# Kernel tuning notes

Hardware: AMD Instinct MI355X
Metric: run time of the kernel (lower is better)

Reference implementation:

```python
import jax, jax.numpy as jnp
import numpy as np

VOCAB, TAGS, EDIM, HDIM = 50000, 9, 256, 512
H = HDIM // 2  # per-direction LSTM hidden
B, S = 64, 512


def setup_inputs() -> dict:
    key = jax.random.key(0)
    ks = jax.random.split(key, 16)
    sc = 0.05
    inp = {
        'sentence_batch': jax.random.randint(ks[0], (B, S), 0, VOCAB),
        'tags_batch': jax.random.randint(ks[1], (B, S), 0, TAGS),
        'mask': jnp.ones((B, S), dtype=bool),
        'emb': jax.random.normal(ks[2], (VOCAB, EDIM), jnp.float32) * sc,
        'w_ih_f': jax.random.normal(ks[3], (4 * H, EDIM), jnp.float32) * sc,
        'w_hh_f': jax.random.normal(ks[4], (4 * H, H), jnp.float32) * sc,
        'b_ih_f': jnp.zeros((4 * H,), jnp.float32),
        'b_hh_f': jnp.zeros((4 * H,), jnp.float32),
        'w_ih_b': jax.random.normal(ks[5], (4 * H, EDIM), jnp.float32) * sc,
        'w_hh_b': jax.random.normal(ks[6], (4 * H, H), jnp.float32) * sc,
        'b_ih_b': jnp.zeros((4 * H,), jnp.float32),
        'b_hh_b': jnp.zeros((4 * H,), jnp.float32),
        'w_out': jax.random.normal(ks[7], (TAGS, HDIM), jnp.float32) * sc,
        'b_out': jnp.zeros((TAGS,), jnp.float32),
        'start_trans': jax.random.uniform(ks[8], (TAGS,), jnp.float32, -0.1, 0.1),
        'end_trans': jax.random.uniform(ks[9], (TAGS,), jnp.float32, -0.1, 0.1),
        'trans': jax.random.uniform(ks[10], (TAGS, TAGS), jnp.float32, -0.1, 0.1),
    }
    return inp


def _lstm_dir(x, w_ih, w_hh, b_ih, b_hh):
    # x: [B,S,E] -> [B,S,H], torch gate order (i,f,g,o)
    b, h = x.shape[0], w_hh.shape[1]
    xg = jnp.einsum('bse,ge->bsg', x, w_ih) + b_ih + b_hh  # precompute input gates

    def step(carry, xg_t):
        hprev, cprev = carry
        g = xg_t + hprev @ w_hh.T
        i, f, gg, o = jnp.split(g, 4, axis=-1)
        c = jax.nn.sigmoid(f) * cprev + jax.nn.sigmoid(i) * jnp.tanh(gg)
        hnew = jax.nn.sigmoid(o) * jnp.tanh(c)
        return (hnew, c), hnew

    init = (jnp.zeros((b, h), x.dtype), jnp.zeros((b, h), x.dtype))
    _, hs = jax.lax.scan(step, init, jnp.swapaxes(xg, 0, 1))
    return jnp.swapaxes(hs, 0, 1)


def _crf_nll(emissions, tags, mask, start_trans, end_trans, trans):
    # emissions [B,S,T], tags [B,S], mask [B,S] bool. torchcrf llh, reduction='mean'.
    b, s, t = emissions.shape
    mf = mask.astype(emissions.dtype)
    # numerator score
    em_sc = jnp.take_along_axis(emissions, tags[..., None], axis=-1)[..., 0]  # [B,S]
    tr_sc = trans[tags[:, :-1], tags[:, 1:]]  # [B,S-1]
    score = start_trans[tags[:, 0]] + em_sc[:, 0]
    score = score + jnp.sum((tr_sc + em_sc[:, 1:]) * mf[:, 1:], axis=-1)
    seq_ends = jnp.sum(mask.astype(jnp.int32), axis=1) - 1
    last_tags = jnp.take_along_axis(tags, seq_ends[:, None], axis=1)[:, 0]
    score = score + end_trans[last_tags]
    # partition via forward algorithm (scan over time)
    alpha0 = start_trans[None, :] + emissions[:, 0]  # [B,T]

    def step(alpha, inputs):
        em_t, m_t = inputs  # [B,T], [B]
        nxt = jax.nn.logsumexp(alpha[:, :, None] + trans[None] + em_t[:, None, :], axis=1)
        alpha = jnp.where(m_t[:, None], nxt, alpha)
        return alpha, None

    em_tm = jnp.swapaxes(emissions[:, 1:], 0, 1)  # [S-1,B,T]
    m_tm = jnp.swapaxes(mask[:, 1:], 0, 1)  # [S-1,B]
    alpha, _ = jax.lax.scan(step, alpha0, (em_tm, m_tm))
    logZ = jax.nn.logsumexp(alpha + end_trans[None, :], axis=-1)
    llh = score - logZ
    return -jnp.mean(llh)


def reference(sentence_batch, tags_batch, mask, emb,
              w_ih_f, w_hh_f, b_ih_f, b_hh_f,
              w_ih_b, w_hh_b, b_ih_b, b_hh_b,
              w_out, b_out, start_trans, end_trans, trans):
    x = emb[sentence_batch]  # [B,S,E]
    hf = _lstm_dir(x, w_ih_f, w_hh_f, b_ih_f, b_hh_f)
    hb = _lstm_dir(x[:, ::-1], w_ih_b, w_hh_b, b_ih_b, b_hh_b)[:, ::-1]
    feats = jnp.concatenate([hf, hb], axis=-1) @ w_out.T + b_out  # [B,S,TAGS]
    return _crf_nll(feats, tags_batch, mask, start_trans, end_trans, trans)
```

## Files before the change

kernel.cpp:

```cpp
#include <hip/hip_runtime.h>
#include <stdint.h>

typedef unsigned short u16;
typedef __attribute__((ext_vector_type(4))) float f32x4;
typedef __attribute__((ext_vector_type(8))) short short8;
typedef __attribute__((ext_vector_type(8))) int v8i;

#define OFF_BIAS   ((size_t)0)
#define OFF_WFRAG  ((size_t)8192)
#define OFF_HHIST  ((size_t)1048576)
#define OFF_FEATS  ((size_t)34603008)
#define OFF_XG     ((size_t)37748736)
#define OFF_XBF    ((size_t)171966464)
#define OFF_WBF    ((size_t)188743680)

__device__ __forceinline__ float bf2f(u16 h) {
  union { uint32_t u; float f; } v; v.u = ((uint32_t)h) << 16; return v.f;
}
__device__ __forceinline__ float bfh(uint32_t wrd, int hh) {
  return bf2f((u16)(wrd >> (16 * hh)));
}
__device__ __forceinline__ uint32_t cvtpk_bf16(float lo, float hi) {
  uint32_t r;
  asm("v_cvt_pk_bf16_f32 %0, %1, %2" : "=v"(r) : "v"(lo), "v"(hi));
  return r;
}
__device__ __forceinline__ uint32_t f2u(float f) {
  union { float f; uint32_t u; } v; v.f = f; return v.u;
}
__device__ __forceinline__ float u2f(uint32_t u) {
  union { uint32_t u; float f; } v; v.u = u; return v.f;
}
__device__ __forceinline__ float pl32_lo(float a, float b) {
  auto pr = __builtin_amdgcn_permlane32_swap(f2u(a), f2u(b), false, false);
  return u2f(((const uint32_t*)&pr)[0]);
}
__device__ __forceinline__ float pl32_hi(float a, float b) {
  auto pr = __builtin_amdgcn_permlane32_swap(f2u(a), f2u(b), false, false);
  return u2f(((const uint32_t*)&pr)[1]);
}
__device__ __forceinline__ short8 pack8(f32x4 a, f32x4 b) {
  union { short8 s; uint32_t u[4]; } r;
  r.u[0] = cvtpk_bf16(a[0], a[1]);
  r.u[1] = cvtpk_bf16(a[2], a[3]);
  r.u[2] = cvtpk_bf16(b[0], b[1]);
  r.u[3] = cvtpk_bf16(b[2], b[3]);
  return r.s;
}

__global__ void bias_kernel(const float* __restrict__ bihf, const float* __restrict__ bhhf,
                            const float* __restrict__ bihb, const float* __restrict__ bhhb,
                            float* __restrict__ bias) {
  int n = blockIdx.x * 256 + threadIdx.x;
  if (n < 1024) bias[n] = bihf[n] + bhhf[n];
  else          bias[n] = bihb[n - 1024] + bhhb[n - 1024];
}

__global__ void __launch_bounds__(256) pack_kernel(
    const int* __restrict__ sent, const float* __restrict__ emb,
    const float* __restrict__ wihf, const float* __restrict__ wihb,
    u16* __restrict__ xbf, u16* __restrict__ wbf)
{
  int gid = blockIdx.x * 256 + threadIdx.x;
  if (gid < 1048576) {
    const int tok = gid >> 5;
    const int c8 = (gid & 31) * 8;
    const int t = sent[tok];
    const float* src = emb + (size_t)t * 256 + c8;
    f32x4 a0 = *(const f32x4*)(src);
    f32x4 a1 = *(const f32x4*)(src + 4);
    *(short8*)(xbf + (size_t)tok * 256 + c8) = pack8(a0, a1);
  } else if (gid < 1114112) {
    const int g2 = gid - 1048576;
    const int row = g2 >> 5;
    const int c8 = (g2 & 31) * 8;
    const float* W = (row < 1024) ? wihf : wihb;
    const float* src = W + (size_t)(row & 1023) * 256 + c8;
    f32x4 a0 = *(const f32x4*)(src);
    f32x4 a1 = *(const f32x4*)(src + 4);
    *(short8*)(wbf + (size_t)row * 256 + c8) = pack8(a0, a1);
  }
}

__global__ void wfrag_prep_kernel(const float* __restrict__ whhf,
                                  const float* __restrict__ whhb,
                                  uint8_t* __restrict__ wfrag) {
  int gid = blockIdx.x * 256 + threadIdx.x;
  const int l    = gid & 63;
  const int kt   = (gid >> 6) & 7;
  const int gate = (gid >> 9) & 3;
  const int ubi  = (gid >> 11) & 1;
  const int w    = (gid >> 12) & 7;
  const int d    = (gid >> 15) & 1;
  const float* W = d ? whhb : whhf;
  const int n = l & 15, q = l >> 4;
  const int row = gate * 256 + w * 32 + ubi * 16 + n;
  uint32_t out[2] = {0u, 0u};
  #pragma unroll
  for (int jj = 0; jj < 4; ++jj) {
    const int k0 = kt * 32 + q * 8 + jj * 2;
    const int k1 = k0 + 1;
    const int u0 = (k0 >> 5) * 32 + (k0 & 1) * 16 + ((k0 & 31) >> 1);
    const int u1 = (k1 >> 5) * 32 + (k1 & 1) * 16 + ((k1 & 31) >> 1);
    const float f0 = W[(size_t)row * 256 + u0] * 16.0f;
    const float f1 = W[(size_t)row * 256 + u1] * 16.0f;
    const int pk = __builtin_amdgcn_cvt_pk_fp8_f32(f0, f1, 0, false);
    out[jj >> 1] |= (uint32_t)(pk & 0xffff) << (16 * (jj & 1));
  }
  const int p = kt >> 2, cc = kt & 3;
  const size_t addr =
      ((((size_t)((d * 8 + w) * 2 + ubi) * 4 + gate) * 2 + p) * 64 + l) * 32 + (size_t)cc * 8;
  *(uint2*)(wfrag + addr) = make_uint2(out[0], out[1]);
}

__global__ void __launch_bounds__(256) xg_gemm_kernel(
    const u16* __restrict__ xbf, const u16* __restrict__ wbf,
    const float* __restrict__ bias, u16* __restrict__ xgf)
{
  extern __shared__ char smem[];
  u16*   Al    = (u16*)smem;
  u16*   Bl    = (u16*)(smem + 34816);
  float* biasl = (float*)(smem + 69632);

  const int tid = threadIdx.x;
  const int d  = blockIdx.x >> 3, u0 = (blockIdx.x & 7) * 32;
  const int g  = blockIdx.y >> 6, qb = (blockIdx.y >> 4) & 3, s0 = (blockIdx.y & 15) * 32;

  if (tid < 128)
    biasl[tid] = bias[d * 1024 + (tid >> 5) * 256 + u0 + (tid & 31)];
  __syncthreads();

  f32x4 acc[4][4];
  #pragma unroll
  for (int i = 0; i < 4; ++i)
    #pragma unroll
    for (int j = 0; j < 4; ++j) acc[i][j] = (f32x4){0.f, 0.f, 0.f, 0.f};

  const int wv = tid >> 6, l = tid & 63;
  const int mh = (wv >> 1) * 64, nh = (wv & 1) * 64;
  const int fr = l & 15, fq = l >> 4;
  const int rr = tid >> 1, c0 = (tid & 1) * 64;

  const int xrow = (g * 16 + qb * 4 + (rr & 3)) * 512 + s0 + (rr >> 2);
  const int wrow = d * 1024 + (rr >> 5) * 256 + u0 + (rr & 31);

  for (int kc = 0; kc < 2; ++kc) {
    const int k0 = kc * 128;
    const u16* as = xbf + (size_t)xrow * 256 + k0 + c0;
    const u16* bs = wbf + (size_t)wrow * 256 + k0 + c0;
    u16* adst = Al + rr * 136 + c0;
    u16* bdst = Bl + rr * 136 + c0;
    #pragma unroll
    for (int gdx = 0; gdx < 8; ++gdx) {
      *(short8*)(adst + gdx * 8) = *(const short8*)(as + gdx * 8);
      *(short8*)(bdst + gdx * 8) = *(const short8*)(bs + gdx * 8);
    }
    __syncthreads();
    #pragma unroll
    for (int ks = 0; ks < 4; ++ks) {
      short8 af[4], bfr[4];
      #pragma unroll
      for (int i = 0; i < 4; ++i)
        af[i] = *(const short8*)(Al + (mh + i * 16 + fr) * 136 + ks * 32 + fq * 8);
      #pragma unroll
      for (int j = 0; j < 4; ++j)
        bfr[j] = *(const short8*)(Bl + (nh + j * 16 + fr) * 136 + ks * 32 + fq * 8);
      #pragma unroll
      for (int i = 0; i < 4; ++i)
        #pragma unroll
        for (int j = 0; j < 4; ++j)
          acc[i][j] = __builtin_amdgcn_mfma_f32_16x16x32_bf16(af[i], bfr[j], acc[i][j], 0, 0, 0);
    }
    __syncthreads();
  }

  const float LOG2E = 1.4426950408889634f;
  const int g0 = nh >> 5;
  const float sA = (g0 == 2) ? (2.0f * LOG2E) : (-LOG2E);
  const int mh4 = mh >> 2;
  const int g8 = g * 2 + (qb >> 1);
  const int qh = qb & 1;
  u16* xbase = xgf + (size_t)(d * 8 + g8) * 4194304;
  #pragma unroll
  for (int i = 0; i < 4; ++i) {
    const int s = s0 + mh4 + i * 4 + fq;
    #pragma unroll
    for (int nsub = 0; nsub < 2; ++nsub) {
      const int j0 = nsub, j1 = nsub + 2;
      const int cA = nh + j0 * 16 + fr, cB = nh + j1 * 16 + fr;
      const int tid2 = (u0 >> 5) * 64 + ((nsub << 1) | qh) * 16 + fr;
      float vA[4], vB[4];
      #pragma unroll
      for (int r = 0; r < 4; ++r) {
        vA[r] = (acc[i][j0][r] + biasl[cA]) * sA;
        vB[r] = (acc[i][j1][r] + biasl[cB]) * (-LOG2E);
      }
      union { short8 s8; uint32_t u[4]; } sv;
      sv.u[0] = cvtpk_bf16(vA[0], vA[1]);
      sv.u[1] = cvtpk_bf16(vA[2], vA[3]);
      sv.u[2] = cvtpk_bf16(vB[0], vB[1]);
      sv.u[3] = cvtpk_bf16(vB[2], vB[3]);
      *(short8*)(xbase + (size_t)s * 8192 + tid2 * 16 + g0 * 4) = sv.s8;
    }
  }
}

template<int CB, int PW>
__device__ __forceinline__ void lstm_step(
    int T, int d, int l, int q, int n, int w,
    const v8i (&wvr)[2][4][2], float (&cst)[4],
    uint4& X0, uint4& X1,
    uint8_t* hx, const u16* xsl, u16* hhb)
{
  const int t_eff = d ? (511 - T) : T;
  const int qh = q & 1;

  int tn = T + 2; if (tn > 511) tn = 511;
  const int sn = d ? (511 - tn) : tn;
  const uint4* pf = (const uint4*)(xsl + (size_t)sn * 8192);
  const uint4 P0 = pf[0], P1 = pf[1];

  const uint8_t* hr = hx + CB * 4224 + (l & 15) * 264 + q * 8;
  const int2 b0 = *(const int2*)(hr +   0);
  const int2 b1 = *(const int2*)(hr +  32);
  const int2 b2 = *(const int2*)(hr +  64);
  const int2 b3 = *(const int2*)(hr +  96);
  const int2 b4 = *(const int2*)(hr + 128);
  const int2 b5 = *(const int2*)(hr + 160);
  const int2 b6 = *(const int2*)(hr + 192);
  const int2 b7 = *(const int2*)(hr + 224);
  const v8i A0 = (v8i){b0.x, b0.y, b1.x, b1.y, b2.x, b2.y, b3.x, b3.y};
  const v8i A1 = (v8i){b4.x, b4.y, b5.x, b5.y, b6.x, b6.y, b7.x, b7.y};

  f32x4 acc[2][4];
  #pragma unroll
  for (int ubi = 0; ubi < 2; ++ubi)
    #pragma unroll
    for (int gate = 0; gate < 4; ++gate) {
      f32x4 a = (f32x4){0.f, 0.f, 0.f, 0.f};
      a = __builtin_amdgcn_mfma_scale_f32_16x16x128_f8f6f4(
              A0, wvr[ubi][gate][0], a, 0, 0, 0, 0x7f7f7f7f, 0, 0x7f7f7f7f);
      a = __builtin_amdgcn_mfma_scale_f32_16x16x128_f8f6f4(
              A1, wvr[ubi][gate][1], a, 0, 0, 0, 0x7f7f7f7f, 0, 0x7f7f7f7f);
      acc[ubi][gate] = a;
    }

  f32x4 accs[4];
  #pragma unroll
  for (int gate = 0; gate < 4; ++gate)
    #pragma unroll
    for (int r = 0; r < 4; ++r)
      accs[gate][r] = pl32_lo(acc[0][gate][r], acc[1][gate][r]);

  const float Sm = -0.0056355275f;
  const float Sg =  0.0112710550f;
  const float K2 =  2.8853900818f;
  float hval[4];
  #pragma unroll
  for (int r = 0; r < 4; ++r) {
    const uint32_t wi = (r < 2) ? X0.x : X0.y;
    const uint32_t wf = (r < 2) ? X0.z : X0.w;
    const uint32_t wg = (r < 2) ? X1.x : X1.y;
    const uint32_t wo = (r < 2) ? X1.z : X1.w;
    const int hp = r & 1;
    const float argi = fmaf(accs[0][r], Sm, bfh(wi, hp));
    const float argf = fmaf(accs[1][r], Sm, bfh(wf, hp));
    const float argg = fmaf(accs[2][r], Sg, bfh(wg, hp));
    const float argo = fmaf(accs[3][r], Sm, bfh(wo, hp));
    const float Ei = __builtin_amdgcn_exp2f(argi);
    const float Ef = __builtin_amdgcn_exp2f(argf);
    const float Eg = __builtin_amdgcn_exp2f(argg);
    const float Eo = __builtin_amdgcn_exp2f(argo);
    const float pf_ = 1.0f + Ef, pi_ = 1.0f + Ei, pg_ = 1.0f + Eg;
    const float P  = pi_ * pg_;
    const float rD = __builtin_amdgcn_rcpf(P * pf_);
    const float num = fmaf(cst[r], P, fmaf(Eg, pf_, -pf_));
    const float c   = num * rD;
    cst[r] = c;
    const float E2 = __builtin_amdgcn_exp2f(c * K2);
    const float rQ = __builtin_amdgcn_rcpf((1.0f + E2) * (1.0f + Eo));
    hval[r] = fmaf(E2, rQ, -rQ);
  }

  float ho[4];
  #pragma unroll
  for (int r = 0; r < 4; ++r) ho[r] = pl32_hi(hval[r], hval[r]);
  if (q < 2) {
    uint8_t* hw = hx + PW * 4224 + w * 32 + 2 * n;
    #pragma unroll
    for (int r = 0; r < 4; ++r) {
      const int pk = __builtin_amdgcn_cvt_pk_fp8_f32(hval[r] * 16.0f,
                                                     ho[r] * 16.0f, 0, false);
      *(u16*)(hw + (q * 4 + r) * 264) = (u16)(pk & 0xffff);
    }
  }

  asm volatile("s_waitcnt lgkmcnt(0)" ::: "memory");
  __builtin_amdgcn_s_barrier();
  __builtin_amdgcn_sched_barrier(0);

  {
    u16* hhs = hhb + (size_t)t_eff * 256;
    const uint32_t pb01 = cvtpk_bf16(hval[0], hval[1]);
    const uint32_t pb23 = cvtpk_bf16(hval[2], hval[3]);
    hhs[(size_t)(qh * 4 + 0) * 131072] = (u16)(pb01 & 0xffffu);
    hhs[(size_t)(qh * 4 + 1) * 131072] = (u16)(pb01 >> 16);
    hhs[(size_t)(qh * 4 + 2) * 131072] = (u16)(pb23 & 0xffffu);
    hhs[(size_t)(qh * 4 + 3) * 131072] = (u16)(pb23 >> 16);
  }

  X0 = P0; X1 = P1;
}

__global__ void __launch_bounds__(512, 2) lstm_kernel(
    const u16* __restrict__ xgf, const uint8_t* __restrict__ wfrag,
    u16* __restrict__ hhist)
{
  __shared__ uint8_t hx[2 * 16 * 264];

  const int tid = threadIdx.x;
  const int bid = blockIdx.x;
  const int d = bid >> 3, g8 = bid & 7;
  const int w = tid >> 6, l = tid & 63;
  const int n = l & 15, q = l >> 4;

  v8i wvr[2][4][2];
  {
    const uint8_t* wb = wfrag + (size_t)(d * 8 + w) * 32768;
    #pragma unroll
    for (int ubi = 0; ubi < 2; ++ubi)
      #pragma unroll
      for (int gate = 0; gate < 4; ++gate)
        #pragma unroll
        for (int p = 0; p < 2; ++p) {
          const uint8_t* src = wb + ((size_t)(((ubi * 4 + gate) * 2 + p) * 64 + l)) * 32;
          const uint4 lo = *(const uint4*)(src);
          const uint4 hi = *(const uint4*)(src + 16);
          wvr[ubi][gate][p] = (v8i){(int)lo.x, (int)lo.y, (int)lo.z, (int)lo.w,
                                    (int)hi.x, (int)hi.y, (int)hi.z, (int)hi.w};
        }
  }

  for (int i = tid; i < 2112; i += 512) ((uint32_t*)hx)[i] = 0u;

  const u16* xsl = xgf + (size_t)(d * 8 + g8) * 4194304 + (size_t)tid * 16;
  float cst[4] = {};
  u16* hhb = hhist + ((size_t)(d * 64 + g8 * 8) * 512) * 256 + (w * 32 + (q >> 1) * 16 + n);

  uint4 X0, X1, Y0, Y1;
  {
    const uint4* p0 = (const uint4*)(xsl + (size_t)(d ? 511 : 0) * 8192);
    X0 = p0[0]; X1 = p0[1];
    const uint4* p1 = (const uint4*)(xsl + (size_t)(d ? 510 : 1) * 8192);
    Y0 = p1[0]; Y1 = p1[1];
  }
  __syncthreads();

  for (int tt = 0; tt < 512; tt += 2) {
    lstm_step<0, 1>(tt,     d, l, q, n, w, wvr, cst, X0, X1, hx, xsl, hhb);
    lstm_step<1, 0>(tt + 1, d, l, q, n, w, wvr, cst, Y0, Y1, hx, xsl, hhb);
  }
}

__global__ void __launch_bounds__(256) proj_kernel(
    const u16* __restrict__ hhist, const float* __restrict__ w_out,
    const float* __restrict__ b_out, float* __restrict__ feats)
{
  __shared__ float wsm[9 * 512];
  __shared__ float bsm[9];
  const int tid = threadIdx.x;
  for (int i = tid; i < 4608; i += 256) wsm[i] = w_out[i];
  if (tid < 9) bsm[tid] = b_out[tid];
  __syncthreads();

  const int wv = tid >> 6, l = tid & 63;
  const int gw = blockIdx.x * 4 + wv;
  const int jb = l * 8;
  const int dd = jb >> 8;
  const int jloc = jb & 255;

  for (int qq = 0; qq < 8; ++qq) {
    const int pos = gw * 8 + qq;
    const int b = pos >> 9, s = pos & 511;
    const u16* hp = hhist + ((size_t)(dd * 64 + b) * 512 + s) * 256 + jloc;
    short8 hv8 = *(const short8*)hp;
    float hf[8];
    #pragma unroll
    for (int j = 0; j < 8; ++j) hf[j] = bf2f((u16)hv8[j]);
    float pt[9];
    #pragma unroll
    for (int tg2 = 0; tg2 < 9; ++tg2) {
      const float* wr = wsm + tg2 * 512 + jb;
      float a = 0.f;
      #pragma unroll
      for (int j = 0; j < 8; ++j) a = fmaf(hf[j], wr[j], a);
      pt[tg2] = a;
    }
    #pragma unroll
    for (int tg2 = 0; tg2 < 9; ++tg2)
      #pragma unroll
      for (int off = 32; off; off >>= 1)
        pt[tg2] += __shfl_xor(pt[tg2], off, 64);
    if (l == 0) {
      float* fo = feats + (size_t)pos * 9;
      #pragma unroll
      for (int tg2 = 0; tg2 < 9; ++tg2) fo[tg2] = pt[tg2] + bsm[tg2];
    }
  }
}

__global__ void __launch_bounds__(64) crf_kernel(
    const float* __restrict__ feats, const int* __restrict__ tags,
    const float* __restrict__ strans, const float* __restrict__ etrans,
    const float* __restrict__ trans, float* out)
{
  __shared__ float em[512 * 9];
  __shared__ float tr[81];
  __shared__ int   tg[512];
  const int b = blockIdx.x, l = threadIdx.x;
  const float* fb = feats + (size_t)b * 512 * 9;
  for (int i = l; i < 4608; i += 64) em[i] = fb[i];
  for (int i = l; i < 512; i += 64) tg[i] = tags[b * 512 + i];
  if (l < 81) tr[l] = trans[l];
  __syncthreads();

  float sc = 0.f;
  for (int s = 1 + l; s < 512; s += 64)
    sc += tr[tg[s - 1] * 9 + tg[s]] + em[s * 9 + tg[s]];
  #pragma unroll
  for (int off = 32; off; off >>= 1) sc += __shfl_xor(sc, off, 64);
  const float score = sc + strans[tg[0]] + em[tg[0]] + etrans[tg[511]];

  const int jj = (l < 9) ? l : 0;
  float al = (l < 9) ? (strans[l] + em[l]) : -1e30f;
  for (int t = 1; t < 512; ++t) {
    float ai[9];
    #pragma unroll
    for (int i = 0; i < 9; ++i) ai[i] = __shfl(al, i, 64);
    float m = ai[0];
    #pragma unroll
    for (int i = 1; i < 9; ++i) m = fmaxf(m, ai[i]);
    float ssum = 0.f;
    #pragma unroll
    for (int i = 0; i < 9; ++i) ssum += __expf(ai[i] + tr[i * 9 + jj] - m);
    al = em[t * 9 + jj] + m + __logf(ssum);
  }
  float v = (l < 9) ? (al + etrans[l]) : -3.0e38f;
  float m2 = v;
  #pragma unroll
  for (int off = 32; off; off >>= 1) m2 = fmaxf(m2, __shfl_xor(m2, off, 64));
  float ex = (l < 9) ? __expf(v - m2) : 0.f;
  #pragma unroll
  for (int off = 32; off; off >>= 1) ex += __shfl_xor(ex, off, 64);
  const float logZ = m2 + __logf(ex);
  if (l == 0) atomicAdd(out, -(score - logZ) * (1.0f / 64.0f));
}

extern "C" void kernel_launch(void* const* d_in, const int* in_sizes, int n_in,
                              void* d_out, int out_size, void* d_ws, size_t ws_size,
                              hipStream_t stream) {
  (void)in_sizes; (void)n_in; (void)out_size; (void)ws_size;
  const int*   sent = (const int*)d_in[0];
  const int*   tags = (const int*)d_in[1];
  const float* emb  = (const float*)d_in[3];
  const float* wihf = (const float*)d_in[4];
  const float* whhf = (const float*)d_in[5];
  const float* bihf = (const float*)d_in[6];
  const float* bhhf = (const float*)d_in[7];
  const float* wihb = (const float*)d_in[8];
  const float* whhb = (const float*)d_in[9];
  const float* bihb = (const float*)d_in[10];
  const float* bhhb = (const float*)d_in[11];
  const float* wout = (const float*)d_in[12];
  const float* bout = (const float*)d_in[13];
  const float* strn = (const float*)d_in[14];
  const float* etrn = (const float*)d_in[15];
  const float* trn  = (const float*)d_in[16];

  char* ws = (char*)d_ws;
  float*   biasb = (float*)(ws + OFF_BIAS);
  uint8_t* wfrag = (uint8_t*)(ws + OFF_WFRAG);
  u16*     hhist = (u16*)(ws + OFF_HHIST);
  float*   feats = (float*)(ws + OFF_FEATS);
  u16*     xgf   = (u16*)(ws + OFF_XG);
  u16*     xbf   = (u16*)(ws + OFF_XBF);
  u16*     wbf   = (u16*)(ws + OFF_WBF);
  float*   out   = (float*)d_out;

  hipMemsetAsync(d_out, 0, sizeof(float), stream);

  hipFuncSetAttribute(reinterpret_cast<const void*>(xg_gemm_kernel),
                      hipFuncAttributeMaxDynamicSharedMemorySize, 70656);

  bias_kernel<<<8, 256, 0, stream>>>(bihf, bhhf, bihb, bhhb, biasb);
  pack_kernel<<<4352, 256, 0, stream>>>(sent, emb, wihf, wihb, xbf, wbf);
  wfrag_prep_kernel<<<128, 256, 0, stream>>>(whhf, whhb, wfrag);
  xg_gemm_kernel<<<dim3(16, 256), 256, 70656, stream>>>(xbf, wbf, biasb, xgf);
  lstm_kernel<<<16, 512, 0, stream>>>(xgf, wfrag, hhist);
  proj_kernel<<<1024, 256, 0, stream>>>(hhist, wout, bout, feats);
  crf_kernel<<<64, 64, 0, stream>>>(feats, tags, strn, etrn, trn, out);
}
```

Baseline: 1.032 ms.

## Split LSTM batch across twice as many workgroups with half rows per block

The recurrent LSTM kernel now launches 32 workgroups instead of 16, each handling 4 batch rows per direction instead of 8. A permlane16 swap redistributes MFMA outputs so each lane does the gate math for 2 elements instead of 4. The xg GEMM output layout is changed to match the new per-block slices. This shortens the serial per-step elementwise work and spreads the recurrence over more CUs, at the cost of duplicated weight-register loads and the MFMA work still being issued with padded rows.

```diff
diff --git a/kernel.cpp b/kernel.cpp
--- a/kernel.cpp
+++ b/kernel.cpp
@@ -38,6 +38,16 @@
 __device__ __forceinline__ float pl32_hi(float a, float b) {
   auto pr = __builtin_amdgcn_permlane32_swap(f2u(a), f2u(b), false, false);
   return u2f(((const uint32_t*)&pr)[1]);
+}
+__device__ __forceinline__ float pl16_bcast(float x) {
+#if __has_builtin(__builtin_amdgcn_permlane16_swap)
+  auto pr = __builtin_amdgcn_permlane16_swap(f2u(x), f2u(x), false, false);
+  return u2f(((const uint32_t*)&pr)[0]);
+#else
+  uint32_t a = f2u(x), b = f2u(x);
+  asm("v_permlane16_swap_b32 %0, %1" : "+v"(a), "+v"(b));
+  return u2f(a);
+#endif
 }
 __device__ __forceinline__ short8 pack8(f32x4 a, f32x4 b) {
   union { short8 s; uint32_t u[4]; } r;
@@ -178,29 +188,28 @@
   const int g0 = nh >> 5;
   const float sA = (g0 == 2) ? (2.0f * LOG2E) : (-LOG2E);
   const int mh4 = mh >> 2;
-  const int g8 = g * 2 + (qb >> 1);
-  const int qh = qb & 1;
-  u16* xbase = xgf + (size_t)(d * 8 + g8) * 4194304;
+  const int g16 = g * 4 + qb;
+  u16* xbase = xgf + (size_t)(d * 16 + g16) * 2097152;
   #pragma unroll
   for (int i = 0; i < 4; ++i) {
     const int s = s0 + mh4 + i * 4 + fq;
     #pragma unroll
     for (int nsub = 0; nsub < 2; ++nsub) {
-      const int j0 = nsub, j1 = nsub + 2;
-      const int cA = nh + j0 * 16 + fr, cB = nh + j1 * 16 + fr;
-      const int tid2 = (u0 >> 5) * 64 + ((nsub << 1) | qh) * 16 + fr;
+      const int cA = nh + nsub * 16 + fr, cB = nh + (nsub + 2) * 16 + fr;
       float vA[4], vB[4];
       #pragma unroll
       for (int r = 0; r < 4; ++r) {
-        vA[r] = (acc[i][j0][r] + biasl[cA]) * sA;
-        vB[r] = (acc[i][j1][r] + biasl[cB]) * (-LOG2E);
+        vA[r] = (acc[i][nsub][r] + biasl[cA]) * sA;
+        vB[r] = (acc[i][nsub + 2][r] + biasl[cB]) * (-LOG2E);
       }
-      union { short8 s8; uint32_t u[4]; } sv;
-      sv.u[0] = cvtpk_bf16(vA[0], vA[1]);
-      sv.u[1] = cvtpk_bf16(vA[2], vA[3]);
-      sv.u[2] = cvtpk_bf16(vB[0], vB[1]);
-      sv.u[3] = cvtpk_bf16(vB[2], vB[3]);
-      *(short8*)(xbase + (size_t)s * 8192 + tid2 * 16 + g0 * 4) = sv.s8;
+      #pragma unroll
+      for (int p = 0; p < 2; ++p) {
+        uint2 sv;
+        sv.x = cvtpk_bf16(vA[p * 2], vA[p * 2 + 1]);
+        sv.y = cvtpk_bf16(vB[p * 2], vB[p * 2 + 1]);
+        const int tid2 = (u0 >> 5) * 64 + ((nsub << 1) | p) * 16 + fr;
+        *(uint2*)(xbase + (size_t)s * 4096 + tid2 * 8 + g0 * 2) = sv;
+      }
     }
   }
 }
@@ -208,17 +217,15 @@
 template<int CB, int PW>
 __device__ __forceinline__ void lstm_step(
     int T, int d, int l, int q, int n, int w,
-    const v8i (&wvr)[2][4][2], float (&cst)[4],
-    uint4& X0, uint4& X1,
+    const v8i (&wvr)[2][4][2], float (&cst)[2],
+    uint4& X0,
     uint8_t* hx, const u16* xsl, u16* hhb)
 {
   const int t_eff = d ? (511 - T) : T;
-  const int qh = q & 1;
 
   int tn = T + 2; if (tn > 511) tn = 511;
   const int sn = d ? (511 - tn) : tn;
-  const uint4* pf = (const uint4*)(xsl + (size_t)sn * 8192);
-  const uint4 P0 = pf[0], P1 = pf[1];
+  const uint4 P0 = *(const uint4*)(xsl + (size_t)sn * 4096);
 
   const uint8_t* hr = hx + CB * 4224 + (l & 15) * 264 + q * 8;
   const int2 b0 = *(const int2*)(hr +   0);
@@ -252,21 +259,25 @@
     for (int r = 0; r < 4; ++r)
       accs[gate][r] = pl32_lo(acc[0][gate][r], acc[1][gate][r]);
 
+  float a2[4][2];
+  #pragma unroll
+  for (int gate = 0; gate < 4; ++gate)
+    #pragma unroll
+    for (int j = 0; j < 2; ++j) {
+      const float t1 = pl16_bcast(accs[gate][2 + j]);
+      a2[gate][j] = (q & 1) ? t1 : accs[gate][j];
+    }
+
   const float Sm = -0.0056355275f;
   const float Sg =  0.0112710550f;
   const float K2 =  2.8853900818f;
-  float hval[4];
-  #pragma unroll
-  for (int r = 0; r < 4; ++r) {
-    const uint32_t wi = (r < 2) ? X0.x : X0.y;
-    const uint32_t wf = (r < 2) ? X0.z : X0.w;
-    const uint32_t wg = (r < 2) ? X1.x : X1.y;
-    const uint32_t wo = (r < 2) ? X1.z : X1.w;
-    const int hp = r & 1;
-    const float argi = fmaf(accs[0][r], Sm, bfh(wi, hp));
-    const float argf = fmaf(accs[1][r], Sm, bfh(wf, hp));
-    const float argg = fmaf(accs[2][r], Sg, bfh(wg, hp));
-    const float argo = fmaf(accs[3][r], Sm, bfh(wo, hp));
+  float hval[2];
+  #pragma unroll
+  for (int j = 0; j < 2; ++j) {
+    const float argi = fmaf(a2[0][j], Sm, bfh(X0.x, j));
+    const float argf = fmaf(a2[1][j], Sm, bfh(X0.y, j));
+    const float argg = fmaf(a2[2][j], Sg, bfh(X0.z, j));
+    const float argo = fmaf(a2[3][j], Sm, bfh(X0.w, j));
     const float Ei = __builtin_amdgcn_exp2f(argi);
     const float Ef = __builtin_amdgcn_exp2f(argf);
     const float Eg = __builtin_amdgcn_exp2f(argg);
@@ -274,25 +285,23 @@
     const float pf_ = 1.0f + Ef, pi_ = 1.0f + Ei, pg_ = 1.0f + Eg;
     const float P  = pi_ * pg_;
     const float rD = __builtin_amdgcn_rcpf(P * pf_);
-    const float num = fmaf(cst[r], P, fmaf(Eg, pf_, -pf_));
+    const float num = fmaf(cst[j], P, fmaf(Eg, pf_, -pf_));
     const float c   = num * rD;
-    cst[r] = c;
+    cst[j] = c;
     const float E2 = __builtin_amdgcn_exp2f(c * K2);
     const float rQ = __builtin_amdgcn_rcpf((1.0f + E2) * (1.0f + Eo));
-    hval[r] = fmaf(E2, rQ, -rQ);
-  }
-
-  float ho[4];
-  #pragma unroll
-  for (int r = 0; r < 4; ++r) ho[r] = pl32_hi(hval[r], hval[r]);
+    hval[j] = fmaf(E2, rQ, -rQ);
+  }
+
+  const float ho0 = pl32_hi(hval[0], hval[0]);
+  const float ho1 = pl32_hi(hval[1], hval[1]);
   if (q < 2) {
     uint8_t* hw = hx + PW * 4224 + w * 32 + 2 * n;
-    #pragma unroll
-    for (int r = 0; r < 4; ++r) {
-      const int pk = __builtin_amdgcn_cvt_pk_fp8_f32(hval[r] * 16.0f,
-                                                     ho[r] * 16.0f, 0, false);
-      *(u16*)(hw + (q * 4 + r) * 264) = (u16)(pk & 0xffff);
-    }
+    const int m0 = (q & 1) * 2;
+    const int pk0 = __builtin_amdgcn_cvt_pk_fp8_f32(hval[0] * 16.0f, ho0 * 16.0f, 0, false);
+    const int pk1 = __builtin_amdgcn_cvt_pk_fp8_f32(hval[1] * 16.0f, ho1 * 16.0f, 0, false);
+    *(u16*)(hw + (m0)     * 264) = (u16)(pk0 & 0xffff);
+    *(u16*)(hw + (m0 + 1) * 264) = (u16)(pk1 & 0xffff);
   }
 
   asm volatile("s_waitcnt lgkmcnt(0)" ::: "memory");
@@ -301,15 +310,13 @@
 
   {
     u16* hhs = hhb + (size_t)t_eff * 256;
-    const uint32_t pb01 = cvtpk_bf16(hval[0], hval[1]);
-    const uint32_t pb23 = cvtpk_bf16(hval[2], hval[3]);
-    hhs[(size_t)(qh * 4 + 0) * 131072] = (u16)(pb01 & 0xffffu);
-    hhs[(size_t)(qh * 4 + 1) * 131072] = (u16)(pb01 >> 16);
-    hhs[(size_t)(qh * 4 + 2) * 131072] = (u16)(pb23 & 0xffffu);
-    hhs[(size_t)(qh * 4 + 3) * 131072] = (u16)(pb23 >> 16);
-  }
-
-  X0 = P0; X1 = P1;
+    const uint32_t pb = cvtpk_bf16(hval[0], hval[1]);
+    const int m0 = (q & 1) * 2;
+    hhs[(size_t)(m0)     * 131072] = (u16)(pb & 0xffffu);
+    hhs[(size_t)(m0 + 1) * 131072] = (u16)(pb >> 16);
+  }
+
+  X0 = P0;
 }
 
 __global__ void __launch_bounds__(512, 2) lstm_kernel(
@@ -320,7 +327,7 @@
 
   const int tid = threadIdx.x;
   const int bid = blockIdx.x;
-  const int d = bid >> 3, g8 = bid & 7;
+  const int d = bid >> 4, g16 = bid & 15;
   const int w = tid >> 6, l = tid & 63;
   const int n = l & 15, q = l >> 4;
 
@@ -343,22 +350,18 @@
 
   for (int i = tid; i < 2112; i += 512) ((uint32_t*)hx)[i] = 0u;
 
-  const u16* xsl = xgf + (size_t)(d * 8 + g8) * 4194304 + (size_t)tid * 16;
-  float cst[4] = {};
-  u16* hhb = hhist + ((size_t)(d * 64 + g8 * 8) * 512) * 256 + (w * 32 + (q >> 1) * 16 + n);
-
-  uint4 X0, X1, Y0, Y1;
-  {
-    const uint4* p0 = (const uint4*)(xsl + (size_t)(d ? 511 : 0) * 8192);
-    X0 = p0[0]; X1 = p0[1];
-    const uint4* p1 = (const uint4*)(xsl + (size_t)(d ? 510 : 1) * 8192);
-    Y0 = p1[0]; Y1 = p1[1];
-  }
+  const u16* xsl = xgf + (size_t)(d * 16 + g16) * 2097152 + (size_t)tid * 8;
+  float cst[2] = {};
+  u16* hhb = hhist + ((size_t)(d * 64 + g16 * 4) * 512) * 256 + (w * 32 + (q >> 1) * 16 + n);
+
+  uint4 X0, Y0;
+  X0 = *(const uint4*)(xsl + (size_t)(d ? 511 : 0) * 4096);
+  Y0 = *(const uint4*)(xsl + (size_t)(d ? 510 : 1) * 4096);
   __syncthreads();
 
   for (int tt = 0; tt < 512; tt += 2) {
-    lstm_step<0, 1>(tt,     d, l, q, n, w, wvr, cst, X0, X1, hx, xsl, hhb);
-    lstm_step<1, 0>(tt + 1, d, l, q, n, w, wvr, cst, Y0, Y1, hx, xsl, hhb);
+    lstm_step<0, 1>(tt,     d, l, q, n, w, wvr, cst, X0, hx, xsl, hhb);
+    lstm_step<1, 0>(tt + 1, d, l, q, n, w, wvr, cst, Y0, hx, xsl, hhb);
   }
 }
 
@@ -496,7 +499,7 @@
   pack_kernel<<<4352, 256, 0, stream>>>(sent, emb, wihf, wihb, xbf, wbf);
   wfrag_prep_kernel<<<128, 256, 0, stream>>>(whhf, whhb, wfrag);
   xg_gemm_kernel<<<dim3(16, 256), 256, 70656, stream>>>(xbf, wbf, biasb, xgf);
-  lstm_kernel<<<16, 512, 0, stream>>>(xgf, wfrag, hhist);
+  lstm_kernel<<<32, 512, 0, stream>>>(xgf, wfrag, hhist);
   proj_kernel<<<1024, 256, 0, stream>>>(hhist, wout, bout, feats);
   crf_kernel<<<64, 64, 0, stream>>>(feats, tags, strn, etrn, trn, out);
 }
```

Result: faster. 946.5 us (-8.3%).
